# Kernel tuning notes

Hardware: AMD Instinct MI355X
Metric: run time of the kernel (lower is better)

Reference implementation:

```python
import jax, jax.numpy as jnp
import numpy as np

B, S = 16, 512
VD, TD, H, NH = 768, 768, 1024, 16
HD = H // NH
MAXREL = 128
THRESH = 2.0 / 3.0


def _bitlinear(x, W, b):
    # BitNet b1.58 eval-mode: ternary-quantize weights, rescale, dense matmul
    s = jnp.clip(jnp.mean(jnp.abs(W)), 1e-5, 1000.0)
    wn = jnp.clip(W / s, -10.0, 10.0)
    q = jnp.where(wn > THRESH, 1.0, jnp.where(wn < -THRESH, -1.0, 0.0))
    return x @ (q * s).T + b


def _ln(x, g, b, eps=1e-5):
    m = jnp.mean(x, axis=-1, keepdims=True)
    v = jnp.mean((x - m) ** 2, axis=-1, keepdims=True)
    return (x - m) * jax.lax.rsqrt(v + eps) * g + b


def setup_inputs() -> dict:
    key = jax.random.key(0)
    ks = jax.random.split(key, 10)
    def n(k, shape, std=0.02):
        return jax.random.normal(k, shape, dtype=jnp.float32) * std
    return dict(
        vision_features=jax.random.normal(ks[0], (B, VD), dtype=jnp.float32),
        text_features=jax.random.normal(ks[1], (B, S, TD), dtype=jnp.float32),
        W_vp=n(ks[2], (H, VD)), b_vp=jnp.zeros((H,), jnp.float32),
        W_tp=n(ks[3], (H, TD)), b_tp=jnp.zeros((H,), jnp.float32),
        W_tqkv=n(ks[4], (3 * H, H)), b_tqkv=jnp.zeros((3 * H,), jnp.float32),
        W_vout=n(ks[5], (H, H)), b_vout=jnp.zeros((H,), jnp.float32),
        W_tout=n(ks[6], (H, H)), b_tout=jnp.zeros((H,), jnp.float32),
        g_tn=jnp.ones((H,), jnp.float32), be_tn=jnp.zeros((H,), jnp.float32),
        g_i2t=jnp.ones((H,), jnp.float32), be_i2t=jnp.zeros((H,), jnp.float32),
        g_t2i=jnp.ones((H,), jnp.float32), be_t2i=jnp.zeros((H,), jnp.float32),
        alpha_i2t=jnp.zeros((1,), jnp.float32),
        alpha_t2i=jnp.zeros((1,), jnp.float32),
        rel_embed=n(ks[7], (2 * MAXREL + 1, NH)),
        text_mask=jnp.ones((B, S), dtype=bool),
    )


def reference(vision_features, text_features, W_vp, b_vp, W_tp, b_tp,
              W_tqkv, b_tqkv, W_vout, b_vout, W_tout, b_tout,
              g_tn, be_tn, g_i2t, be_i2t, g_t2i, be_t2i,
              alpha_i2t, alpha_t2i, rel_embed, text_mask):
    scale = HD ** -0.5
    vision_proj = _bitlinear(vision_features, W_vp, b_vp)            # [B,H]
    text_proj = _bitlinear(text_features, W_tp, b_tp)                # [B,S,H]

    # --- text self-attention with relative-position bias ---
    qkv = _bitlinear(_ln(text_proj, g_tn, be_tn), W_tqkv, b_tqkv)    # [B,S,3H]
    qkv = qkv.reshape(B, S, 3, NH, HD).transpose(2, 0, 3, 1, 4)      # [3,B,nh,S,hd]
    q, k, v = qkv[0], qkv[1], qkv[2]
    attn = jnp.einsum('bhqd,bhkd->bhqk', q, k) * scale
    coords = jnp.arange(S)
    rel = jnp.clip(coords[:, None] - coords[None, :], -MAXREL, MAXREL) + MAXREL
    attn = attn + rel_embed[rel].transpose(2, 0, 1)[None]            # +[1,nh,S,S]
    attn = jnp.where(text_mask[:, None, None, :], attn, -1e9)
    attn = jax.nn.softmax(attn, axis=-1)
    text_self = jnp.einsum('bhqk,bhkd->bhqd', attn, v)
    text_self = text_self.transpose(0, 2, 1, 3).reshape(B, S, H)
    text_self = text_proj + text_self                                # residual

    # --- image -> text cross-attention (vision token queries text) ---
    vq = jnp.broadcast_to(vision_proj[:, None], (B, S, H))
    vq = vq.reshape(B, S, NH, HD).transpose(0, 2, 1, 3)              # [B,nh,S,hd]
    tkv = text_self.reshape(B, S, NH, HD).transpose(0, 2, 1, 3)      # [B,nh,S,hd]
    i2t = jnp.einsum('bhqd,bhkd->bhqk', vq, tkv) * scale
    i2t = jnp.where(text_mask[:, None, None, :], i2t, -1e9)
    i2t = jax.nn.softmax(i2t, axis=-1)
    i2t_out = jnp.einsum('bhqk,bhkd->bhqd', i2t, tkv)
    i2t_out = i2t_out.transpose(0, 2, 1, 3).reshape(B, S, H).mean(axis=1)
    i2t_out = _ln(i2t_out, g_i2t, be_i2t)                            # [B,H]
    fused_vision = vision_proj + alpha_i2t * _bitlinear(i2t_out, W_vout, b_vout)

    # --- text -> image cross-attention (text queries single vision token) ---
    tq = text_self.reshape(B, S, NH, HD).transpose(0, 2, 1, 3)       # [B,nh,S,hd]
    vkv = vision_proj.reshape(B, 1, NH, HD).transpose(0, 2, 1, 3)    # [B,nh,1,hd]
    t2i = jnp.einsum('bhqd,bhkd->bhqk', tq, vkv) * scale             # [B,nh,S,1]
    t2i = jax.nn.softmax(t2i, axis=-1)
    t2i_out = jnp.einsum('bhqk,bhkd->bhqd', t2i, vkv)
    t2i_out = t2i_out.transpose(0, 2, 1, 3).reshape(B, S, H)
    t2i_out = _ln(t2i_out, g_t2i, be_t2i)
    fused_text = text_self + alpha_t2i * _bitlinear(t2i_out, W_tout, b_tout)

    return fused_vision, fused_text
```

## Files before the change

### kernel.cpp

```cpp
#include <hip/hip_runtime.h>
#include <cstdint>

#define B_   16
#define S_   512
#define VD_  768
#define TD_  768
#define H_   1024
#define NH_  16
#define HD_  64
#define H3_  3072

typedef __attribute__((ext_vector_type(8))) short bf16x8;
typedef __attribute__((ext_vector_type(4))) float f32x4;

__device__ __forceinline__ float b2f(unsigned short h) {
  union { unsigned u; float f; } x; x.u = ((unsigned)h) << 16; return x.f;
}
__device__ __forceinline__ unsigned short f2b(float f) {
  union { float f; unsigned u; } x; x.f = f;
  unsigned r = x.u + 0x7fffu + ((x.u >> 16) & 1u);
  return (unsigned short)(r >> 16);
}
__device__ __forceinline__ unsigned cvt_pk_bf16(float lo, float hi) {
  unsigned r;
  __asm__("v_cvt_pk_bf16_f32 %0, %1, %2" : "=v"(r) : "v"(lo), "v"(hi));
  return r;
}
__device__ __forceinline__ float fexp2(float x) {
#if __has_builtin(__builtin_amdgcn_exp2f)
  return __builtin_amdgcn_exp2f(x);
#else
  return exp2f(x);
#endif
}

__device__ __forceinline__ void gload_lds16(const void* g, void* lds) {
  __builtin_amdgcn_global_load_lds(
      (const __attribute__((address_space(1))) unsigned int*)g,
      (__attribute__((address_space(3))) unsigned int*)lds, 16, 0, 0);
}
__device__ __forceinline__ void lds_wave_fence() {
  __asm__ __volatile__("s_waitcnt lgkmcnt(0)" ::: "memory");
}

__global__ __launch_bounds__(256) void k_abssum_cvt(const float* __restrict__ w0, int n0,
                                                    const float* __restrict__ w1, int n1,
                                                    const float* __restrict__ w2, int n2,
                                                    const float* __restrict__ w3, int n3,
                                                    const float* __restrict__ w4, int n4,
                                                    double* __restrict__ partials,
                                                    const float* __restrict__ cvt_in,
                                                    unsigned short* __restrict__ cvt_out,
                                                    int cvt_n4) {
  int y = blockIdx.y;
  if (y == 5) {
    for (int i = blockIdx.x * 256 + threadIdx.x; i < cvt_n4; i += 128 * 256) {
      float4 v = ((const float4*)cvt_in)[i];
      ushort4 o; o.x = f2b(v.x); o.y = f2b(v.y); o.z = f2b(v.z); o.w = f2b(v.w);
      ((ushort4*)cvt_out)[i] = o;
    }
    return;
  }
  const float* w = y == 0 ? w0 : y == 1 ? w1 : y == 2 ? w2 : y == 3 ? w3 : w4;
  int n4q = (y == 0 ? n0 : y == 1 ? n1 : y == 2 ? n2 : y == 3 ? n3 : n4) >> 2;
  double s = 0.0;
  for (int i = blockIdx.x * 256 + threadIdx.x; i < n4q; i += 128 * 256) {
    float4 v = ((const float4*)w)[i];
    s += (double)fabsf(v.x) + (double)fabsf(v.y) + (double)fabsf(v.z) + (double)fabsf(v.w);
  }
#pragma unroll
  for (int off = 32; off > 0; off >>= 1) s += __shfl_down(s, off, 64);
  __shared__ double red[4];
  if ((threadIdx.x & 63) == 0) red[threadIdx.x >> 6] = s;
  __syncthreads();
  if (threadIdx.x == 0)
    partials[y * 128 + blockIdx.x] = red[0] + red[1] + red[2] + red[3];
}

__global__ __launch_bounds__(512) void k_sumfin(const double* __restrict__ partials,
                                                double* __restrict__ sums) {
  int wave = threadIdx.x >> 6, lane = threadIdx.x & 63;
  if (wave >= 5) return;
  double s = partials[wave * 128 + lane] + partials[wave * 128 + 64 + lane];
#pragma unroll
  for (int off = 32; off > 0; off >>= 1) s += __shfl_down(s, off, 64);
  if (lane == 0) sums[wave] = s;
}

__global__ __launch_bounds__(256) void k_quant5(const float* __restrict__ w0, int n0,
                                                const float* __restrict__ w1, int n1,
                                                const float* __restrict__ w2, int n2,
                                                const float* __restrict__ w3, int n3,
                                                const float* __restrict__ w4, int n4,
                                                unsigned short* __restrict__ q0,
                                                unsigned short* __restrict__ q1,
                                                unsigned short* __restrict__ q2,
                                                unsigned short* __restrict__ q3,
                                                unsigned short* __restrict__ q4,
                                                const double* __restrict__ sum,
                                                float* __restrict__ s_out) {
  int y = blockIdx.y;
  const float* w = y == 0 ? w0 : y == 1 ? w1 : y == 2 ? w2 : y == 3 ? w3 : w4;
  unsigned short* q = y == 0 ? q0 : y == 1 ? q1 : y == 2 ? q2 : y == 3 ? q3 : q4;
  int n = y == 0 ? n0 : y == 1 ? n1 : y == 2 ? n2 : y == 3 ? n3 : n4;
  double s = fmin(fmax(sum[y] / (double)n, 1e-5), 1000.0);
  if (blockIdx.x == 0 && threadIdx.x == 0) s_out[y] = (float)s;
  int i = blockIdx.x * 256 + threadIdx.x;
  if (i < n) {
    double wn = (double)w[i] / s;
    unsigned short o = 0;
    if (wn > (2.0 / 3.0)) o = 0x3F80u;
    else if (wn < -(2.0 / 3.0)) o = 0xBF80u;
    q[i] = o;
  }
}

__global__ __launch_bounds__(256) void k_rowmat(const float* __restrict__ A,
                                                const unsigned short* __restrict__ W,
                                                const float* __restrict__ sptr,
                                                const float* __restrict__ bias,
                                                float* __restrict__ Cf,
                                                unsigned short* __restrict__ Cb,
                                                const float* __restrict__ resid,
                                                const float* __restrict__ alpha,
                                                int N, int K) {
  const int t = threadIdx.x, lane = t & 63;
  const int w_idx = blockIdx.x * 4 + (t >> 6);
  const int m = w_idx / N, n = w_idx - m * N;
  const int Kper = K >> 6;
  const float* a = A + (size_t)m * K + lane * Kper;
  const unsigned short* w = W + (size_t)n * K + lane * Kper;
  float acc = 0.f;
  for (int k = 0; k < Kper; k += 4) {
    float4 av = *(const float4*)(a + k);
    ushort4 wv = *(const ushort4*)(w + k);
    acc += av.x * b2f(wv.x) + av.y * b2f(wv.y) + av.z * b2f(wv.z) + av.w * b2f(wv.w);
  }
#pragma unroll
  for (int off = 32; off > 0; off >>= 1) acc += __shfl_down(acc, off, 64);
  if (lane == 0) {
    float v = acc * sptr[0] + bias[n];
    if (resid) v = resid[w_idx] + alpha[0] * v;
    Cf[w_idx] = v;
    if (Cb) Cb[w_idx] = f2b(v);
  }
}

__global__ __launch_bounds__(256) void k_ln(const float* __restrict__ x,
                                            const float* __restrict__ g,
                                            const float* __restrict__ be,
                                            float* __restrict__ of,
                                            unsigned short* __restrict__ ob) {
  int row = blockIdx.x, t = threadIdx.x;
  const float4* xr = (const float4*)(x + (size_t)row * H_);
  float4 v = xr[t];
  float s = v.x + v.y + v.z + v.w;
  float s2 = v.x * v.x + v.y * v.y + v.z * v.z + v.w * v.w;
#pragma unroll
  for (int off = 32; off > 0; off >>= 1) { s += __shfl_down(s, off, 64); s2 += __shfl_down(s2, off, 64); }
  __shared__ float rs[4], rs2[4];
  if ((t & 63) == 0) { rs[t >> 6] = s; rs2[t >> 6] = s2; }
  __syncthreads();
  s = rs[0] + rs[1] + rs[2] + rs[3];
  s2 = rs2[0] + rs2[1] + rs2[2] + rs2[3];
  float mean = s * (1.0f / H_);
  float var = s2 * (1.0f / H_) - mean * mean;
  float rstd = rsqrtf(var + 1e-5f);
  const float4 gv = ((const float4*)g)[t];
  const float4 bv = ((const float4*)be)[t];
  float4 o;
  o.x = (v.x - mean) * rstd * gv.x + bv.x;
  o.y = (v.y - mean) * rstd * gv.y + bv.y;
  o.z = (v.z - mean) * rstd * gv.z + bv.z;
  o.w = (v.w - mean) * rstd * gv.w + bv.w;
  if (of) ((float4*)(of + (size_t)row * H_))[t] = o;
  if (ob) {
    ushort4 ou; ou.x = f2b(o.x); ou.y = f2b(o.y); ou.z = f2b(o.z); ou.w = f2b(o.w);
    ((ushort4*)(ob + (size_t)row * H_))[t] = ou;
  }
}

template <int OUTB, int VT>
__global__ __launch_bounds__(256) void k_gemm(const unsigned short* __restrict__ A,
                                              const unsigned short* __restrict__ W,
                                              const float* __restrict__ sptr,
                                              const float* __restrict__ bias,
                                              float* __restrict__ Cf,
                                              unsigned short* __restrict__ Cb,
                                              unsigned short* __restrict__ vt,
                                              int M, int N, int K) {
  __shared__ __align__(16) unsigned short As[2][128 * 64];
  __shared__ __align__(16) unsigned short Bs[2][128 * 64];
  const int t = threadIdx.x, wave = t >> 6, lane = t & 63, quad = lane >> 4, l16 = lane & 15;
  const int bm = blockIdx.y * 128, bn = blockIdx.x * 128;
  const int wm = (wave >> 1) * 64, wn = (wave & 1) * 64;
  const int srow = lane >> 3, kc = (lane & 7) ^ srow;
  f32x4 acc[4][4];
#pragma unroll
  for (int i = 0; i < 4; ++i)
#pragma unroll
    for (int j = 0; j < 4; ++j) acc[i][j] = f32x4{0.f, 0.f, 0.f, 0.f};

  auto stage = [&](int kt, int buf) {
    const int k0 = kt * 64;
#pragma unroll
    for (int c = 0; c < 4; ++c) {
      int row = wave * 32 + c * 8 + srow;
      gload_lds16(A + (size_t)(bm + row) * K + k0 + kc * 8,
                  &As[buf][(wave * 32 + c * 8) * 64]);
      gload_lds16(W + (size_t)(bn + row) * K + k0 + kc * 8,
                  &Bs[buf][(wave * 32 + c * 8) * 64]);
    }
  };

  const int NT = K >> 6;
  stage(0, 0);
  for (int kt = 0; kt < NT; ++kt) {
    const int cur = kt & 1;
    if (kt + 1 < NT) {
      stage(kt + 1, cur ^ 1);
      __asm__ __volatile__("s_waitcnt vmcnt(8)" ::: "memory");
    } else {
      __asm__ __volatile__("s_waitcnt vmcnt(0)" ::: "memory");
    }
    __asm__ __volatile__("s_barrier" ::: "memory");
#pragma unroll
    for (int ks = 0; ks < 2; ++ks) {
      bf16x8 af[4], bfrg[4];
#pragma unroll
      for (int i = 0; i < 4; ++i) {
        int R = wm + i * 16 + l16;
        af[i] = *(const bf16x8*)&As[cur][R * 64 + (((ks * 4 + quad) ^ (R & 7)) * 8)];
      }
#pragma unroll
      for (int j = 0; j < 4; ++j) {
        int R = wn + j * 16 + l16;
        bfrg[j] = *(const bf16x8*)&Bs[cur][R * 64 + (((ks * 4 + quad) ^ (R & 7)) * 8)];
      }
      __builtin_amdgcn_s_setprio(1);
#pragma unroll
      for (int i = 0; i < 4; ++i)
#pragma unroll
        for (int j = 0; j < 4; ++j)
          acc[i][j] = __builtin_amdgcn_mfma_f32_16x16x32_bf16(af[i], bfrg[j], acc[i][j], 0, 0, 0);
      __builtin_amdgcn_s_setprio(0);
    }
    __asm__ __volatile__("s_barrier" ::: "memory");
  }
  float s = sptr[0];

  if (VT && bn >= 2 * H_) {
    unsigned short* T = (wave < 2) ? &As[0][wave * 1152] : &Bs[0][(wave - 2) * 1152];
    const int h = (bn + wn - 2 * H_) >> 6;
    const int b = (bm + wm) >> 9, s0 = (bm + wm) & (S_ - 1);
    const int chunk0 = lane * 2;
#pragma unroll
    for (int j = 0; j < 4; ++j) {
      int n = bn + wn + j * 16 + l16;
      float bv = bias[n];
#pragma unroll
      for (int i = 0; i < 4; ++i)
#pragma unroll
        for (int r = 0; r < 4; ++r)
          T[l16 * 72 + i * 16 + quad * 4 + r] = f2b(acc[i][j][r] * s + bv);
      lds_wave_fence();
#pragma unroll
      for (int cc = 0; cc < 2; ++cc) {
        int ch = chunk0 + cc, dr = ch >> 3, k8 = ch & 7;
        uint4 val = *(const uint4*)&T[dr * 72 + k8 * 8];
        *(uint4*)(vt + ((size_t)(b * NH_ + h) * HD_ + j * 16 + dr) * S_ + s0 + k8 * 8) = val;
      }
      lds_wave_fence();
    }
    return;
  }

#pragma unroll
  for (int j = 0; j < 4; ++j) {
    int n = bn + wn + j * 16 + l16;
    float bv = bias[n];
#pragma unroll
    for (int i = 0; i < 4; ++i) {
#pragma unroll
      for (int r = 0; r < 4; ++r) {
        int m = bm + wm + i * 16 + quad * 4 + r;
        float v = acc[i][j][r] * s + bv;
        if (OUTB) Cb[(size_t)m * N + n] = f2b(v);
        else      Cf[(size_t)m * N + n] = v;
      }
    }
  }
}

__global__ __launch_bounds__(256) void k_flash(const unsigned short* __restrict__ qkv,
                                               const unsigned short* __restrict__ vt,
                                               const float* __restrict__ tp,
                                               const float* __restrict__ rel,
                                               const float* __restrict__ trow,
                                               const float* __restrict__ a_t2i,
                                               float* __restrict__ out_text,
                                               unsigned short* __restrict__ ts_b) {
  const int qt = blockIdx.x, h = blockIdx.y, b = blockIdx.z;
  __shared__ __align__(16) unsigned short Qs[64 * 64];
  __shared__ __align__(16) unsigned short Ks[2][64 * 64];
  __shared__ __align__(16) unsigned short Vs[2][64 * 64];
  __shared__ __align__(16) unsigned short Ps[4][16 * 72];
  __shared__ float rels[257];
  const int t = threadIdx.x, wave = t >> 6, lane = t & 63, quad = lane >> 4, l16 = lane & 15;
  const int srow = lane >> 3;
  const int kcg = (lane & 7) ^ srow;
  const float LOG2E = 1.4426950408889634f;
  const float SC = 0.125f * LOG2E;

  for (int i = t; i < 257; i += 256) rels[i] = rel[i * NH_ + h] * LOG2E;

  auto stage_kv = [&](int kt, int buf) {
#pragma unroll
    for (int c = 0; c < 2; ++c) {
      int row = (wave * 2 + c) * 8 + srow;
      gload_lds16(qkv + (size_t)(b * S_ + kt * 64 + row) * H3_ + H_ + h * HD_ + kcg * 8,
                  &Ks[buf][(wave * 2 + c) * 512]);
      gload_lds16(vt + ((size_t)(b * NH_ + h) * HD_ + row) * S_ + kt * 64 + kcg * 8,
                  &Vs[buf][(wave * 2 + c) * 512]);
    }
  };

#pragma unroll
  for (int c = 0; c < 2; ++c) {
    int row = (wave * 2 + c) * 8 + srow;
    gload_lds16(qkv + (size_t)(b * S_ + qt * 64 + row) * H3_ + h * HD_ + kcg * 8,
                &Qs[(wave * 2 + c) * 512]);
  }
  stage_kv(0, 0);

  float mrun = -1e30f, lrun = 0.f;
  f32x4 o[4];
#pragma unroll
  for (int j = 0; j < 4; ++j) o[j] = f32x4{0.f, 0.f, 0.f, 0.f};

  bf16x8 aq0, aq1;
  bool qloaded = false;
  const int qg = qt * 64 + wave * 16 + l16;

  for (int kt = 0; kt < 8; ++kt) {
    const int cur = kt & 1;
    __syncthreads();
    if (kt < 7) stage_kv(kt + 1, cur ^ 1);

    if (!qloaded) {
      int R = wave * 16 + l16;
      aq0 = *(const bf16x8*)&Qs[R * 64 + ((quad ^ (R & 7)) * 8)];
      aq1 = *(const bf16x8*)&Qs[R * 64 + (((4 + quad) ^ (R & 7)) * 8)];
      qloaded = true;
    }

    const int dq = qt - kt;
    const bool uni = (dq >= 3) || (dq <= -3);
    const float bu = uni ? rels[dq >= 3 ? 256 : 0] : 0.f;

    float pv[4][4];
#pragma unroll
    for (int j = 0; j < 4; ++j) {
      int R = j * 16 + l16;
      bf16x8 kb0 = *(const bf16x8*)&Ks[cur][R * 64 + ((quad ^ (R & 7)) * 8)];
      bf16x8 kb1 = *(const bf16x8*)&Ks[cur][R * 64 + (((4 + quad) ^ (R & 7)) * 8)];
      f32x4 z = f32x4{0.f, 0.f, 0.f, 0.f};
      z = __builtin_amdgcn_mfma_f32_16x16x32_bf16(kb0, aq0, z, 0, 0, 0);
      z = __builtin_amdgcn_mfma_f32_16x16x32_bf16(kb1, aq1, z, 0, 0, 0);
      if (uni) {
#pragma unroll
        for (int r = 0; r < 4; ++r) pv[j][r] = z[r] * SC + bu;
      } else {
        const int kg0 = kt * 64 + j * 16 + quad * 4;
#pragma unroll
        for (int r = 0; r < 4; ++r) {
          int rix = min(max(qg - kg0 - r, -128), 128) + 128;
          pv[j][r] = z[r] * SC + rels[rix];
        }
      }
    }
    float x = pv[0][0];
#pragma unroll
    for (int j = 0; j < 4; ++j)
#pragma unroll
      for (int r = 0; r < 4; ++r) x = fmaxf(x, pv[j][r]);
    x = fmaxf(x, __shfl_xor(x, 16, 64));
    x = fmaxf(x, __shfl_xor(x, 32, 64));
    if (!__all(x <= mrun)) {
      float mn = fmaxf(mrun, x);
      float al = fexp2(mrun - mn);
      mrun = mn;
      lrun *= al;
      float al0 = __shfl(al, quad * 4 + 0, 64);
      float al1 = __shfl(al, quad * 4 + 1, 64);
      float al2 = __shfl(al, quad * 4 + 2, 64);
      float al3 = __shfl(al, quad * 4 + 3, 64);
#pragma unroll
      for (int jd = 0; jd < 4; ++jd) {
        o[jd][0] *= al0; o[jd][1] *= al1; o[jd][2] *= al2; o[jd][3] *= al3;
      }
    }
    float rsum = 0.f;
#pragma unroll
    for (int j = 0; j < 4; ++j)
#pragma unroll
      for (int r = 0; r < 4; ++r) {
        float p = fexp2(pv[j][r] - mrun);
        pv[j][r] = p;
        rsum += p;
      }
    rsum += __shfl_xor(rsum, 16, 64);
    rsum += __shfl_xor(rsum, 32, 64);
    lrun += rsum;
    unsigned char* psb = (unsigned char*)&Ps[wave][0] + l16 * 144 + quad * 8;
#pragma unroll
    for (int j = 0; j < 4; ++j) {
      uint2 pk;
      pk.x = cvt_pk_bf16(pv[j][0], pv[j][1]);
      pk.y = cvt_pk_bf16(pv[j][2], pv[j][3]);
      *(uint2*)(psb + j * 32) = pk;
    }
    lds_wave_fence();
#pragma unroll
    for (int ks = 0; ks < 2; ++ks) {
      bf16x8 ap = *(const bf16x8*)&Ps[wave][l16 * 72 + ks * 32 + quad * 8];
#pragma unroll
      for (int jd = 0; jd < 4; ++jd) {
        int R = jd * 16 + l16;
        int C = ks * 4 + quad;
        bf16x8 vb = *(const bf16x8*)&Vs[cur][R * 64 + ((C ^ (R & 7)) * 8)];
        o[jd] = __builtin_amdgcn_mfma_f32_16x16x32_bf16(ap, vb, o[jd], 0, 0, 0);
      }
    }
  }
  float a2 = a_t2i[0];
  float il[4];
#pragma unroll
  for (int r = 0; r < 4; ++r) {
    float lr = __shfl(lrun, quad * 4 + r, 64);
    il[r] = 1.0f / lr;
  }
#pragma unroll
  for (int jd = 0; jd < 4; ++jd) {
#pragma unroll
    for (int r = 0; r < 4; ++r) {
      int g = b * S_ + qt * 64 + wave * 16 + quad * 4 + r;
      int col = h * HD_ + jd * 16 + l16;
      float ov = o[jd][r] * il[r];
      float ts = tp[(size_t)g * H_ + col] + ov;
      ts_b[(size_t)g * H_ + col] = f2b(ts);
      out_text[(size_t)g * H_ + col] = ts + a2 * trow[b * H_ + col];
    }
  }
}

__global__ __launch_bounds__(256) void k_i2t(const unsigned short* __restrict__ vp_b,
                                             const unsigned short* __restrict__ ts_b,
                                             float* __restrict__ i2t_out) {
  const int h = blockIdx.x & 15, b = blockIdx.x >> 4;
  __shared__ float sc[512];
  __shared__ float red[4];
  __shared__ float qv[64];
  __shared__ float ored[4][64];
  const int t = threadIdx.x;
  if (t < 64) qv[t] = b2f(vp_b[b * H_ + h * HD_ + t]);
  __syncthreads();
  for (int k = t; k < 512; k += 256) {
    const unsigned short* kr = ts_b + (size_t)(b * S_ + k) * H_ + h * HD_;
    float acc = 0.f;
#pragma unroll
    for (int dc = 0; dc < 8; ++dc) {
      uint4 u = *(const uint4*)(kr + dc * 8);
      const unsigned short* p = (const unsigned short*)&u;
#pragma unroll
      for (int i = 0; i < 8; ++i) acc += qv[dc * 8 + i] * b2f(p[i]);
    }
    sc[k] = acc * 0.125f;
  }
  __syncthreads();
  float m = -1e30f;
  for (int k = t; k < 512; k += 256) m = fmaxf(m, sc[k]);
#pragma unroll
  for (int off = 1; off < 64; off <<= 1) m = fmaxf(m, __shfl_xor(m, off, 64));
  if ((t & 63) == 0) red[t >> 6] = m;
  __syncthreads();
  m = fmaxf(fmaxf(red[0], red[1]), fmaxf(red[2], red[3]));
  __syncthreads();
  float ls = 0.f;
  for (int k = t; k < 512; k += 256) { float p = __expf(sc[k] - m); sc[k] = p; ls += p; }
#pragma unroll
  for (int off = 1; off < 64; off <<= 1) ls += __shfl_xor(ls, off, 64);
  if ((t & 63) == 0) red[t >> 6] = ls;
  __syncthreads();
  float tot = red[0] + red[1] + red[2] + red[3];
  const int d = t & 63, grp = t >> 6;
  float acc = 0.f;
  for (int k = grp; k < 512; k += 4)
    acc += sc[k] * b2f(ts_b[(size_t)(b * S_ + k) * H_ + h * HD_ + d]);
  ored[grp][d] = acc;
  __syncthreads();
  if (t < 64)
    i2t_out[b * H_ + h * HD_ + t] = (ored[0][t] + ored[1][t] + ored[2][t] + ored[3][t]) / tot;
}

extern "C" void kernel_launch(void* const* d_in, const int* in_sizes, int n_in,
                              void* d_out, int out_size, void* d_ws, size_t ws_size,
                              hipStream_t stream) {
  const float* vf     = (const float*)d_in[0];
  const float* tf     = (const float*)d_in[1];
  const float* W_vp   = (const float*)d_in[2];
  const float* b_vp   = (const float*)d_in[3];
  const float* W_tp   = (const float*)d_in[4];
  const float* b_tp   = (const float*)d_in[5];
  const float* W_tqkv = (const float*)d_in[6];
  const float* b_tqkv = (const float*)d_in[7];
  const float* W_vout = (const float*)d_in[8];
  const float* b_vout = (const float*)d_in[9];
  const float* W_tout = (const float*)d_in[10];
  const float* b_tout = (const float*)d_in[11];
  const float* g_tn   = (const float*)d_in[12];
  const float* be_tn  = (const float*)d_in[13];
  const float* g_i2t  = (const float*)d_in[14];
  const float* be_i2t = (const float*)d_in[15];
  const float* g_t2i  = (const float*)d_in[16];
  const float* be_t2i = (const float*)d_in[17];
  const float* a_i2t  = (const float*)d_in[18];
  const float* a_t2i  = (const float*)d_in[19];
  const float* rel    = (const float*)d_in[20];

  size_t off = 0;
  auto alloc = [&](size_t bytes) -> void* {
    void* p = (char*)d_ws + off;
    off += (bytes + 255) & ~(size_t)255;
    return p;
  };
  double* sums     = (double*)alloc(64);
  double* partials = (double*)alloc(5 * 128 * 8);
  float* scales    = (float*)alloc(64);
  unsigned short* q_vp   = (unsigned short*)alloc((size_t)H_ * VD_ * 2);
  unsigned short* q_tp   = (unsigned short*)alloc((size_t)H_ * TD_ * 2);
  unsigned short* q_tqkv = (unsigned short*)alloc((size_t)H3_ * H_ * 2);
  unsigned short* q_vout = (unsigned short*)alloc((size_t)H_ * H_ * 2);
  unsigned short* q_tout = (unsigned short*)alloc((size_t)H_ * H_ * 2);
  unsigned short* tf_b   = (unsigned short*)alloc((size_t)B_ * S_ * TD_ * 2);
  float* text_proj       = (float*)alloc((size_t)B_ * S_ * H_ * 4);
  unsigned short* ln_tp  = (unsigned short*)alloc((size_t)B_ * S_ * H_ * 2);
  unsigned short* qkv    = (unsigned short*)alloc((size_t)B_ * S_ * H3_ * 2);
  unsigned short* vt     = (unsigned short*)alloc((size_t)B_ * NH_ * HD_ * S_ * 2);
  unsigned short* ts_b   = (unsigned short*)alloc((size_t)B_ * S_ * H_ * 2);
  float* vision_proj     = (float*)alloc((size_t)B_ * H_ * 4);
  unsigned short* vp_b   = (unsigned short*)alloc((size_t)B_ * H_ * 2);
  float* ln_t2i_f        = (float*)alloc((size_t)B_ * H_ * 4);
  float* trow            = (float*)alloc((size_t)B_ * H_ * 4);
  float* i2t_out         = (float*)alloc((size_t)B_ * H_ * 4);
  float* ln_i2t_f        = (float*)alloc((size_t)B_ * H_ * 4);

  float* out_vision = (float*)d_out;
  float* out_text   = (float*)d_out + B_ * H_;

  k_abssum_cvt<<<dim3(128, 6), 256, 0, stream>>>(W_vp, H_ * VD_, W_tp, H_ * TD_,
                                                 W_tqkv, H3_ * H_, W_vout, H_ * H_,
                                                 W_tout, H_ * H_, partials,
                                                 tf, tf_b, B_ * S_ * TD_ / 4);
  k_sumfin<<<1, 512, 0, stream>>>(partials, sums);
  k_quant5<<<dim3((H3_ * H_ + 255) / 256, 5), 256, 0, stream>>>(
      W_vp, H_ * VD_, W_tp, H_ * TD_, W_tqkv, H3_ * H_, W_vout, H_ * H_, W_tout, H_ * H_,
      q_vp, q_tp, q_tqkv, q_vout, q_tout, sums, scales);

  k_rowmat<<<(B_ * H_) / 4, 256, 0, stream>>>(vf, q_vp, scales + 0, b_vp,
                                              vision_proj, vp_b, nullptr, nullptr, H_, VD_);
  k_ln<<<B_, 256, 0, stream>>>(vision_proj, g_t2i, be_t2i, ln_t2i_f, nullptr);
  k_rowmat<<<(B_ * H_) / 4, 256, 0, stream>>>(ln_t2i_f, q_tout, scales + 4, b_tout,
                                              trow, nullptr, nullptr, nullptr, H_, H_);

  k_gemm<0, 0><<<dim3(H_ / 128, (B_ * S_) / 128), 256, 0, stream>>>(
      tf_b, q_tp, scales + 1, b_tp, text_proj, nullptr, nullptr, B_ * S_, H_, TD_);
  k_ln<<<B_ * S_, 256, 0, stream>>>(text_proj, g_tn, be_tn, nullptr, ln_tp);
  k_gemm<1, 1><<<dim3(H3_ / 128, (B_ * S_) / 128), 256, 0, stream>>>(
      ln_tp, q_tqkv, scales + 2, b_tqkv, nullptr, qkv, vt, B_ * S_, H3_, H_);
  k_flash<<<dim3(S_ / 64, NH_, B_), 256, 0, stream>>>(qkv, vt, text_proj, rel, trow, a_t2i,
                                                      out_text, ts_b);
  k_i2t<<<B_ * NH_, 256, 0, stream>>>(vp_b, ts_b, i2t_out);
  k_ln<<<B_, 256, 0, stream>>>(i2t_out, g_i2t, be_i2t, ln_i2t_f, nullptr);
  k_rowmat<<<(B_ * H_) / 4, 256, 0, stream>>>(ln_i2t_f, q_vout, scales + 3, b_vout,
                                              out_vision, nullptr, vision_proj, a_i2t, H_, H_);
}
```

Measured before the change: 376.6 us.

## Process all queries of a head per flash block to reuse K/V tiles

Restructures the flash attention kernel so each block of 8 waves handles a whole (batch, head) sequence, with each wave owning 64 query rows as four 16-row groups. K/V tiles are staged once per head instead of once per 64-query tile, cutting global and LDS traffic. The cost is a grid of only 256 blocks and much higher register pressure from four sets of accumulators, which may reduce occupancy and latency hiding.

```diff
diff --git a/kernel.cpp b/kernel.cpp
--- a/kernel.cpp
+++ b/kernel.cpp
@@ -292,19 +292,18 @@
   }
 }
 
-__global__ __launch_bounds__(256) void k_flash(const unsigned short* __restrict__ qkv,
-                                               const unsigned short* __restrict__ vt,
-                                               const float* __restrict__ tp,
-                                               const float* __restrict__ rel,
-                                               const float* __restrict__ trow,
-                                               const float* __restrict__ a_t2i,
-                                               float* __restrict__ out_text,
-                                               unsigned short* __restrict__ ts_b) {
-  const int qt = blockIdx.x, h = blockIdx.y, b = blockIdx.z;
-  __shared__ __align__(16) unsigned short Qs[64 * 64];
+__global__ __launch_bounds__(512, 2) void k_flash(const unsigned short* __restrict__ qkv,
+                                                  const unsigned short* __restrict__ vt,
+                                                  const float* __restrict__ tp,
+                                                  const float* __restrict__ rel,
+                                                  const float* __restrict__ trow,
+                                                  const float* __restrict__ a_t2i,
+                                                  float* __restrict__ out_text,
+                                                  unsigned short* __restrict__ ts_b) {
+  const int h = blockIdx.x, b = blockIdx.y;
   __shared__ __align__(16) unsigned short Ks[2][64 * 64];
   __shared__ __align__(16) unsigned short Vs[2][64 * 64];
-  __shared__ __align__(16) unsigned short Ps[4][16 * 72];
+  __shared__ __align__(16) unsigned short Ps[8][16 * 72];
   __shared__ float rels[257];
   const int t = threadIdx.x, wave = t >> 6, lane = t & 63, quad = lane >> 4, l16 = lane & 15;
   const int srow = lane >> 3;
@@ -312,144 +311,173 @@
   const float LOG2E = 1.4426950408889634f;
   const float SC = 0.125f * LOG2E;
 
-  for (int i = t; i < 257; i += 256) rels[i] = rel[i * NH_ + h] * LOG2E;
+  for (int i = t; i < 257; i += 512) rels[i] = rel[i * NH_ + h] * LOG2E;
 
   auto stage_kv = [&](int kt, int buf) {
-#pragma unroll
-    for (int c = 0; c < 2; ++c) {
-      int row = (wave * 2 + c) * 8 + srow;
-      gload_lds16(qkv + (size_t)(b * S_ + kt * 64 + row) * H3_ + H_ + h * HD_ + kcg * 8,
-                  &Ks[buf][(wave * 2 + c) * 512]);
-      gload_lds16(vt + ((size_t)(b * NH_ + h) * HD_ + row) * S_ + kt * 64 + kcg * 8,
-                  &Vs[buf][(wave * 2 + c) * 512]);
-    }
+    int row = wave * 8 + srow;
+    gload_lds16(qkv + (size_t)(b * S_ + kt * 64 + row) * H3_ + H_ + h * HD_ + kcg * 8,
+                &Ks[buf][(wave * 8) * 64]);
+    gload_lds16(vt + ((size_t)(b * NH_ + h) * HD_ + row) * S_ + kt * 64 + kcg * 8,
+                &Vs[buf][(wave * 8) * 64]);
   };
-
-#pragma unroll
-  for (int c = 0; c < 2; ++c) {
-    int row = (wave * 2 + c) * 8 + srow;
-    gload_lds16(qkv + (size_t)(b * S_ + qt * 64 + row) * H3_ + h * HD_ + kcg * 8,
-                &Qs[(wave * 2 + c) * 512]);
-  }
+  auto stageQ = [&](int chunk, unsigned short* buf) {
+    int row = chunk * 64 + wave * 8 + srow;
+    gload_lds16(qkv + (size_t)(b * S_ + row) * H3_ + h * HD_ + kcg * 8,
+                buf + (wave * 8) * 64);
+  };
+
+  bf16x8 aq0[4], aq1[4];
+  unsigned short* qb0 = &Ks[0][0];
+  unsigned short* qb1 = &Vs[0][0];
+  unsigned short* qb2 = &Ks[1][0];
+  unsigned short* qb3 = &Vs[1][0];
+  stageQ(0, qb0); stageQ(1, qb1); stageQ(2, qb2); stageQ(3, qb3);
+  __syncthreads();
+  if (wave < 4) {
+    const unsigned short* qb = wave == 0 ? qb0 : wave == 1 ? qb1 : wave == 2 ? qb2 : qb3;
+#pragma unroll
+    for (int rg = 0; rg < 4; ++rg) {
+      int R = rg * 16 + l16;
+      aq0[rg] = *(const bf16x8*)&qb[R * 64 + ((quad ^ (R & 7)) * 8)];
+      aq1[rg] = *(const bf16x8*)&qb[R * 64 + (((4 + quad) ^ (R & 7)) * 8)];
+    }
+  }
+  __syncthreads();
+  stageQ(4, qb0); stageQ(5, qb1); stageQ(6, qb2); stageQ(7, qb3);
+  __syncthreads();
+  if (wave >= 4) {
+    const int c = wave - 4;
+    const unsigned short* qb = c == 0 ? qb0 : c == 1 ? qb1 : c == 2 ? qb2 : qb3;
+#pragma unroll
+    for (int rg = 0; rg < 4; ++rg) {
+      int R = rg * 16 + l16;
+      aq0[rg] = *(const bf16x8*)&qb[R * 64 + ((quad ^ (R & 7)) * 8)];
+      aq1[rg] = *(const bf16x8*)&qb[R * 64 + (((4 + quad) ^ (R & 7)) * 8)];
+    }
+  }
+  __syncthreads();
   stage_kv(0, 0);
 
-  float mrun = -1e30f, lrun = 0.f;
-  f32x4 o[4];
-#pragma unroll
-  for (int j = 0; j < 4; ++j) o[j] = f32x4{0.f, 0.f, 0.f, 0.f};
-
-  bf16x8 aq0, aq1;
-  bool qloaded = false;
-  const int qg = qt * 64 + wave * 16 + l16;
+  float mrun[4], lrun[4];
+  f32x4 o[4][4];
+#pragma unroll
+  for (int rg = 0; rg < 4; ++rg) {
+    mrun[rg] = -1e30f; lrun[rg] = 0.f;
+#pragma unroll
+    for (int j = 0; j < 4; ++j) o[rg][j] = f32x4{0.f, 0.f, 0.f, 0.f};
+  }
 
   for (int kt = 0; kt < 8; ++kt) {
     const int cur = kt & 1;
     __syncthreads();
     if (kt < 7) stage_kv(kt + 1, cur ^ 1);
 
-    if (!qloaded) {
-      int R = wave * 16 + l16;
-      aq0 = *(const bf16x8*)&Qs[R * 64 + ((quad ^ (R & 7)) * 8)];
-      aq1 = *(const bf16x8*)&Qs[R * 64 + (((4 + quad) ^ (R & 7)) * 8)];
-      qloaded = true;
-    }
-
-    const int dq = qt - kt;
-    const bool uni = (dq >= 3) || (dq <= -3);
-    const float bu = uni ? rels[dq >= 3 ? 256 : 0] : 0.f;
-
-    float pv[4][4];
-#pragma unroll
-    for (int j = 0; j < 4; ++j) {
-      int R = j * 16 + l16;
-      bf16x8 kb0 = *(const bf16x8*)&Ks[cur][R * 64 + ((quad ^ (R & 7)) * 8)];
-      bf16x8 kb1 = *(const bf16x8*)&Ks[cur][R * 64 + (((4 + quad) ^ (R & 7)) * 8)];
-      f32x4 z = f32x4{0.f, 0.f, 0.f, 0.f};
-      z = __builtin_amdgcn_mfma_f32_16x16x32_bf16(kb0, aq0, z, 0, 0, 0);
-      z = __builtin_amdgcn_mfma_f32_16x16x32_bf16(kb1, aq1, z, 0, 0, 0);
-      if (uni) {
-#pragma unroll
-        for (int r = 0; r < 4; ++r) pv[j][r] = z[r] * SC + bu;
-      } else {
-        const int kg0 = kt * 64 + j * 16 + quad * 4;
+#pragma unroll
+    for (int rg = 0; rg < 4; ++rg) {
+      const int qb_row = wave * 64 + rg * 16;
+      const int dqb = qb_row - kt * 64;
+      const bool uni = (dqb >= 192) || (dqb <= -144);
+      const float bu = uni ? rels[dqb >= 192 ? 256 : 0] : 0.f;
+      const int qg = qb_row + l16;
+
+      float pv[4][4];
+#pragma unroll
+      for (int j = 0; j < 4; ++j) {
+        int R = j * 16 + l16;
+        bf16x8 kb0 = *(const bf16x8*)&Ks[cur][R * 64 + ((quad ^ (R & 7)) * 8)];
+        bf16x8 kb1 = *(const bf16x8*)&Ks[cur][R * 64 + (((4 + quad) ^ (R & 7)) * 8)];
+        f32x4 z = f32x4{0.f, 0.f, 0.f, 0.f};
+        z = __builtin_amdgcn_mfma_f32_16x16x32_bf16(kb0, aq0[rg], z, 0, 0, 0);
+        z = __builtin_amdgcn_mfma_f32_16x16x32_bf16(kb1, aq1[rg], z, 0, 0, 0);
+        if (uni) {
+#pragma unroll
+          for (int r = 0; r < 4; ++r) pv[j][r] = z[r] * SC + bu;
+        } else {
+          const int kg0 = kt * 64 + j * 16 + quad * 4;
+#pragma unroll
+          for (int r = 0; r < 4; ++r) {
+            int rix = min(max(qg - kg0 - r, -128), 128) + 128;
+            pv[j][r] = z[r] * SC + rels[rix];
+          }
+        }
+      }
+      float x = pv[0][0];
+#pragma unroll
+      for (int j = 0; j < 4; ++j)
+#pragma unroll
+        for (int r = 0; r < 4; ++r) x = fmaxf(x, pv[j][r]);
+      x = fmaxf(x, __shfl_xor(x, 16, 64));
+      x = fmaxf(x, __shfl_xor(x, 32, 64));
+      if (!__all(x <= mrun[rg])) {
+        float mn = fmaxf(mrun[rg], x);
+        float al = fexp2(mrun[rg] - mn);
+        mrun[rg] = mn;
+        lrun[rg] *= al;
+        float al0 = __shfl(al, quad * 4 + 0, 64);
+        float al1 = __shfl(al, quad * 4 + 1, 64);
+        float al2 = __shfl(al, quad * 4 + 2, 64);
+        float al3 = __shfl(al, quad * 4 + 3, 64);
+#pragma unroll
+        for (int jd = 0; jd < 4; ++jd) {
+          o[rg][jd][0] *= al0; o[rg][jd][1] *= al1;
+          o[rg][jd][2] *= al2; o[rg][jd][3] *= al3;
+        }
+      }
+      float rsum = 0.f;
+#pragma unroll
+      for (int j = 0; j < 4; ++j)
 #pragma unroll
         for (int r = 0; r < 4; ++r) {
-          int rix = min(max(qg - kg0 - r, -128), 128) + 128;
-          pv[j][r] = z[r] * SC + rels[rix];
+          float p = fexp2(pv[j][r] - mrun[rg]);
+          pv[j][r] = p;
+          rsum += p;
         }
-      }
-    }
-    float x = pv[0][0];
-#pragma unroll
-    for (int j = 0; j < 4; ++j)
-#pragma unroll
-      for (int r = 0; r < 4; ++r) x = fmaxf(x, pv[j][r]);
-    x = fmaxf(x, __shfl_xor(x, 16, 64));
-    x = fmaxf(x, __shfl_xor(x, 32, 64));
-    if (!__all(x <= mrun)) {
-      float mn = fmaxf(mrun, x);
-      float al = fexp2(mrun - mn);
-      mrun = mn;
-      lrun *= al;
-      float al0 = __shfl(al, quad * 4 + 0, 64);
-      float al1 = __shfl(al, quad * 4 + 1, 64);
-      float al2 = __shfl(al, quad * 4 + 2, 64);
-      float al3 = __shfl(al, quad * 4 + 3, 64);
-#pragma unroll
-      for (int jd = 0; jd < 4; ++jd) {
-        o[jd][0] *= al0; o[jd][1] *= al1; o[jd][2] *= al2; o[jd][3] *= al3;
-      }
-    }
-    float rsum = 0.f;
-#pragma unroll
-    for (int j = 0; j < 4; ++j)
+      rsum += __shfl_xor(rsum, 16, 64);
+      rsum += __shfl_xor(rsum, 32, 64);
+      lrun[rg] += rsum;
+      unsigned char* psb = (unsigned char*)&Ps[wave][0] + l16 * 144 + quad * 8;
+#pragma unroll
+      for (int j = 0; j < 4; ++j) {
+        uint2 pk;
+        pk.x = cvt_pk_bf16(pv[j][0], pv[j][1]);
+        pk.y = cvt_pk_bf16(pv[j][2], pv[j][3]);
+        *(uint2*)(psb + j * 32) = pk;
+      }
+      lds_wave_fence();
+#pragma unroll
+      for (int ks = 0; ks < 2; ++ks) {
+        bf16x8 ap = *(const bf16x8*)&Ps[wave][l16 * 72 + ks * 32 + quad * 8];
+#pragma unroll
+        for (int jd = 0; jd < 4; ++jd) {
+          int R = jd * 16 + l16;
+          int C = ks * 4 + quad;
+          bf16x8 vb = *(const bf16x8*)&Vs[cur][R * 64 + ((C ^ (R & 7)) * 8)];
+          o[rg][jd] = __builtin_amdgcn_mfma_f32_16x16x32_bf16(ap, vb, o[rg][jd], 0, 0, 0);
+        }
+      }
+      lds_wave_fence();
+    }
+  }
+  float a2 = a_t2i[0];
+#pragma unroll
+  for (int rg = 0; rg < 4; ++rg) {
+    float il[4];
+#pragma unroll
+    for (int r = 0; r < 4; ++r) {
+      float lr = __shfl(lrun[rg], quad * 4 + r, 64);
+      il[r] = 1.0f / lr;
+    }
+#pragma unroll
+    for (int jd = 0; jd < 4; ++jd) {
 #pragma unroll
       for (int r = 0; r < 4; ++r) {
-        float p = fexp2(pv[j][r] - mrun);
-        pv[j][r] = p;
-        rsum += p;
-      }
-    rsum += __shfl_xor(rsum, 16, 64);
-    rsum += __shfl_xor(rsum, 32, 64);
-    lrun += rsum;
-    unsigned char* psb = (unsigned char*)&Ps[wave][0] + l16 * 144 + quad * 8;
-#pragma unroll
-    for (int j = 0; j < 4; ++j) {
-      uint2 pk;
-      pk.x = cvt_pk_bf16(pv[j][0], pv[j][1]);
-      pk.y = cvt_pk_bf16(pv[j][2], pv[j][3]);
-      *(uint2*)(psb + j * 32) = pk;
-    }
-    lds_wave_fence();
-#pragma unroll
-    for (int ks = 0; ks < 2; ++ks) {
-      bf16x8 ap = *(const bf16x8*)&Ps[wave][l16 * 72 + ks * 32 + quad * 8];
-#pragma unroll
-      for (int jd = 0; jd < 4; ++jd) {
-        int R = jd * 16 + l16;
-        int C = ks * 4 + quad;
-        bf16x8 vb = *(const bf16x8*)&Vs[cur][R * 64 + ((C ^ (R & 7)) * 8)];
-        o[jd] = __builtin_amdgcn_mfma_f32_16x16x32_bf16(ap, vb, o[jd], 0, 0, 0);
-      }
-    }
-  }
-  float a2 = a_t2i[0];
-  float il[4];
-#pragma unroll
-  for (int r = 0; r < 4; ++r) {
-    float lr = __shfl(lrun, quad * 4 + r, 64);
-    il[r] = 1.0f / lr;
-  }
-#pragma unroll
-  for (int jd = 0; jd < 4; ++jd) {
-#pragma unroll
-    for (int r = 0; r < 4; ++r) {
-      int g = b * S_ + qt * 64 + wave * 16 + quad * 4 + r;
-      int col = h * HD_ + jd * 16 + l16;
-      float ov = o[jd][r] * il[r];
-      float ts = tp[(size_t)g * H_ + col] + ov;
-      ts_b[(size_t)g * H_ + col] = f2b(ts);
-      out_text[(size_t)g * H_ + col] = ts + a2 * trow[b * H_ + col];
+        int g = b * S_ + wave * 64 + rg * 16 + quad * 4 + r;
+        int col = h * HD_ + jd * 16 + l16;
+        float ov = o[rg][jd][r] * il[r];
+        float ts = tp[(size_t)g * H_ + col] + ov;
+        ts_b[(size_t)g * H_ + col] = f2b(ts);
+        out_text[(size_t)g * H_ + col] = ts + a2 * trow[b * H_ + col];
+      }
     }
   }
 }
@@ -578,8 +606,8 @@
   k_ln<<<B_ * S_, 256, 0, stream>>>(text_proj, g_tn, be_tn, nullptr, ln_tp);
   k_gemm<1, 1><<<dim3(H3_ / 128, (B_ * S_) / 128), 256, 0, stream>>>(
       ln_tp, q_tqkv, scales + 2, b_tqkv, nullptr, qkv, vt, B_ * S_, H3_, H_);
-  k_flash<<<dim3(S_ / 64, NH_, B_), 256, 0, stream>>>(qkv, vt, text_proj, rel, trow, a_t2i,
-                                                      out_text, ts_b);
+  k_flash<<<dim3(NH_, B_), 512, 0, stream>>>(qkv, vt, text_proj, rel, trow, a_t2i,
+                                             out_text, ts_b);
   k_i2t<<<B_ * NH_, 256, 0, stream>>>(vp_b, ts_b, i2t_out);
   k_ln<<<B_, 256, 0, stream>>>(i2t_out, g_i2t, be_i2t, ln_i2t_f, nullptr);
   k_rowmat<<<(B_ * H_) / 4, 256, 0, stream>>>(ln_i2t_f, q_vout, scales + 3, b_vout,
```

Result: no change. 369.9 us (-1.8%).
